# Kernel optimization log

Measured on AMD Instinct MI355X. Metric: run time of the kernel, lower is better.

The kernel has to match this reference:

```python
import jax, jax.numpy as jnp
import numpy as np

N_NODES = 100000   # number of graph nodes
DEG = 16           # fixed average degree
N_EDGES = N_NODES * DEG  # 1,600,000
D_FEAT = 48        # node feature dim


def setup_inputs() -> dict:
    key = jax.random.key(0)
    k1, k2 = jax.random.split(key)
    X = jax.random.normal(k1, (N_NODES, D_FEAT), dtype=jnp.float32)
    # CSR row offsets for a fixed-degree graph: row i owns edges [i*DEG, (i+1)*DEG)
    row_pointers = jnp.arange(N_NODES + 1, dtype=jnp.int32) * DEG
    # neighbor (source) node index per edge
    column_index = jax.random.randint(k2, (N_EDGES,), 0, N_NODES, dtype=jnp.int32)
    return {"X": X, "row_pointers": row_pointers, "column_index": column_index}


def reference(X, row_pointers, column_index):
    # Unweighted CSR SpMM neighbor aggregation (same math as TCGNN.forward SAG):
    #   out[i] = sum_{e in [row_ptr[i], row_ptr[i+1])} X[column_index[e]]
    n = row_pointers.shape[0] - 1
    e = column_index.shape[0]
    deg = jnp.diff(row_pointers)  # [n] edges per destination row
    # destination row id for every edge (static total length keeps this jit-able)
    row_ids = jnp.repeat(jnp.arange(n, dtype=jnp.int32), deg, total_repeat_length=e)
    gathered = X[column_index]  # [E, D] gather of neighbor features
    return jax.ops.segment_sum(gathered, row_ids, num_segments=n)  # [n, D]
```

## Files before the change

kernel.cpp:

```cpp
#include <hip/hip_runtime.h>


#define N_NODES 100000
#define DEG 16
#define NCHUNK (N_NODES * 4)

__global__ __launch_bounds__(256) void encode_kernel(
    const float4* __restrict__ X,
    uint4* __restrict__ Xq)
{
    int g = blockIdx.x * 256 + threadIdx.x;
    if (g >= NCHUNK) return;
    float4 a = X[g * 3 + 0];
    float4 b = X[g * 3 + 1];
    float4 d = X[g * 3 + 2];
    float x[12] = {a.x, a.y, a.z, a.w, b.x, b.y, b.z, b.w, d.x, d.y, d.z, d.w};

    float m = 0.f;
    #pragma unroll
    for (int j = 0; j < 12; ++j) m = fmaxf(m, fabsf(x[j]));

    int e;
    if (m > 0.f) {
        float t = m * (1.0f / 511.0f);
        e = (int)((__float_as_uint(t) >> 23) & 255u) - 126;
    } else {
        e = -64;
    }
    float inv_s = __uint_as_float((unsigned)(127 - e) << 23);
    unsigned code = (unsigned)(e + 64) & 255u;

    unsigned w[4];
    #pragma unroll
    for (int dw = 0; dw < 4; ++dw) {
        unsigned acc = 0u;
        #pragma unroll
        for (int k = 0; k < 3; ++k) {
            int q = __float2int_rn(x[dw * 3 + k] * inv_s);
            q = max(-511, min(511, q));
            acc |= ((unsigned)q & 1023u) << (10 * k);
        }
        acc |= ((code >> (2 * dw)) & 3u) << 30;
        w[dw] = acc;
    }
    uint4 o; o.x = w[0]; o.y = w[1]; o.z = w[2]; o.w = w[3];
    Xq[g] = o;
}

__global__ __launch_bounds__(256) void sag_q8_kernel(
    const uint4* __restrict__ Xq,
    const int* __restrict__ col,
    float4* __restrict__ out)
{
    const int t = threadIdx.x;
    const int node = blockIdx.x * 32 + (t >> 3);
    const int sub = t & 7;
    const int c = sub & 3;
    const int half = sub >> 2;
    if (node >= N_NODES) return;

    const int4* ip = (const int4*)(col + node * DEG + half * 8);
    int4 v0 = ip[0];
    int4 v1 = ip[1];
    int idx[8] = {v0.x, v0.y, v0.z, v0.w, v1.x, v1.y, v1.z, v1.w};

    uint4 w[8];
    #pragma unroll
    for (int k = 0; k < 8; ++k) {
        w[k] = Xq[((unsigned)idx[k] << 2) + c];
    }

    float acc[12];
    #pragma unroll
    for (int j = 0; j < 12; ++j) acc[j] = 0.f;

    #pragma unroll
    for (int k = 0; k < 8; ++k) {
        unsigned ws[4] = {w[k].x, w[k].y, w[k].z, w[k].w};
        unsigned code = (ws[0] >> 30) | ((ws[1] >> 30) << 2) |
                        ((ws[2] >> 30) << 4) | ((ws[3] >> 30) << 6);
        float s = __uint_as_float((code + 63u) << 23);
        #pragma unroll
        for (int dw = 0; dw < 4; ++dw) {
            unsigned wv = ws[dw];
            int q0 = ((int)(wv << 22)) >> 22;
            int q1 = ((int)(wv << 12)) >> 22;
            int q2 = ((int)(wv <<  2)) >> 22;
            acc[dw * 3 + 0] += (float)q0 * s;
            acc[dw * 3 + 1] += (float)q1 * s;
            acc[dw * 3 + 2] += (float)q2 * s;
        }
    }

    #pragma unroll
    for (int j = 0; j < 12; ++j) acc[j] += __shfl_xor(acc[j], 4);

    float4* o = out + ((long)node * 12 + c * 3);
    if (half == 0) {
        o[0] = make_float4(acc[0], acc[1],  acc[2],  acc[3]);
        o[1] = make_float4(acc[4], acc[5],  acc[6],  acc[7]);
    } else {
        o[2] = make_float4(acc[8], acc[9],  acc[10], acc[11]);
    }
}

__global__ __launch_bounds__(192) void sag_f32_kernel(
    const float4* __restrict__ X,
    const int* __restrict__ col,
    float4* __restrict__ out)
{
    const int t = threadIdx.x;
    const int node = blockIdx.x * 16 + t / 12;
    const int c = t % 12;
    if (node >= N_NODES) return;
    const int4* ip = (const int4*)(col + node * DEG);
    int idx[DEG];
    #pragma unroll
    for (int q = 0; q < 4; ++q) {
        int4 v = ip[q];
        idx[4 * q + 0] = v.x; idx[4 * q + 1] = v.y;
        idx[4 * q + 2] = v.z; idx[4 * q + 3] = v.w;
    }
    float4 acc = make_float4(0.f, 0.f, 0.f, 0.f);
    #pragma unroll
    for (int e = 0; e < DEG; ++e) {
        float4 v = X[idx[e] * 12 + c];
        acc.x += v.x; acc.y += v.y; acc.z += v.z; acc.w += v.w;
    }
    out[node * 12 + c] = acc;
}

extern "C" void kernel_launch(void* const* d_in, const int* in_sizes, int n_in,
                              void* d_out, int out_size, void* d_ws, size_t ws_size,
                              hipStream_t stream) {
    const float4* X = (const float4*)d_in[0];
    const int* col = (const int*)d_in[2];
    float4* out = (float4*)d_out;

    const size_t xq_bytes = (size_t)N_NODES * 64;

    if (ws_size >= xq_bytes) {
        uint4* Xq = (uint4*)d_ws;
        encode_kernel<<<(NCHUNK + 255) / 256, 256, 0, stream>>>(X, Xq);
        const int blocks = (N_NODES + 31) / 32;
        sag_q8_kernel<<<blocks, 256, 0, stream>>>(Xq, col, out);
    } else {
        const int blocks = (N_NODES + 15) / 16;
        sag_f32_kernel<<<blocks, 192, 0, stream>>>(X, col, out);
    }
}
```

Measured before the change: 95.66 us.

## Split quantized gather into two passes by source-node half for cache locality

The aggregation now runs in two launches: the first gathers only neighbors whose index falls in the lower half of the node range, and the second gathers the upper half and adds the first pass's partial sums read back from the output. The goal is to make each pass's random gather working set (half of the 6.4 MB encoded table) fit better in cache. Streaming loads and stores of the inputs, outputs and column indices are marked nontemporal. In exchange, the column indices are read twice, the output is written twice and read once more, and there is an extra launch.

```diff
diff --git a/kernel.cpp b/kernel.cpp
--- a/kernel.cpp
+++ b/kernel.cpp
@@ -4,16 +4,21 @@
 #define N_NODES 100000
 #define DEG 16
 #define NCHUNK (N_NODES * 4)
+#define HALF_SPLIT (N_NODES / 2)
+
+typedef float    f4 __attribute__((ext_vector_type(4)));
+typedef int      i4 __attribute__((ext_vector_type(4)));
+typedef unsigned u4 __attribute__((ext_vector_type(4)));
 
 __global__ __launch_bounds__(256) void encode_kernel(
-    const float4* __restrict__ X,
-    uint4* __restrict__ Xq)
+    const f4* __restrict__ X,
+    u4* __restrict__ Xq)
 {
     int g = blockIdx.x * 256 + threadIdx.x;
     if (g >= NCHUNK) return;
-    float4 a = X[g * 3 + 0];
-    float4 b = X[g * 3 + 1];
-    float4 d = X[g * 3 + 2];
+    f4 a = __builtin_nontemporal_load(X + g * 3 + 0);
+    f4 b = __builtin_nontemporal_load(X + g * 3 + 1);
+    f4 d = __builtin_nontemporal_load(X + g * 3 + 2);
     float x[12] = {a.x, a.y, a.z, a.w, b.x, b.y, b.z, b.w, d.x, d.y, d.z, d.w};
 
     float m = 0.f;
@@ -43,14 +48,15 @@
         acc |= ((code >> (2 * dw)) & 3u) << 30;
         w[dw] = acc;
     }
-    uint4 o; o.x = w[0]; o.y = w[1]; o.z = w[2]; o.w = w[3];
-    Xq[g] = o;
+    u4 o = {w[0], w[1], w[2], w[3]};
+    __builtin_nontemporal_store(o, Xq + g);
 }
 
-__global__ __launch_bounds__(256) void sag_q8_kernel(
-    const uint4* __restrict__ Xq,
+template<int H>
+__global__ __launch_bounds__(256) void sag_q8_pass(
+    const u4* __restrict__ Xq,
     const int* __restrict__ col,
-    float4* __restrict__ out)
+    f4* __restrict__ out)
 {
     const int t = threadIdx.x;
     const int node = blockIdx.x * 32 + (t >> 3);
@@ -59,15 +65,32 @@
     const int half = sub >> 2;
     if (node >= N_NODES) return;
 
-    const int4* ip = (const int4*)(col + node * DEG + half * 8);
-    int4 v0 = ip[0];
-    int4 v1 = ip[1];
+    f4* o = out + ((long)node * 12 + c * 3);
+
+    f4 p0 = {0.f, 0.f, 0.f, 0.f};
+    f4 p1 = p0, p2 = p0;
+    if (H == 1) {
+        if (half == 0) {
+            p0 = __builtin_nontemporal_load(o + 0);
+            p1 = __builtin_nontemporal_load(o + 1);
+        } else {
+            p2 = __builtin_nontemporal_load(o + 2);
+        }
+    }
+
+    const i4* ip = (const i4*)(col + node * DEG + half * 8);
+    i4 v0 = __builtin_nontemporal_load(ip + 0);
+    i4 v1 = __builtin_nontemporal_load(ip + 1);
     int idx[8] = {v0.x, v0.y, v0.z, v0.w, v1.x, v1.y, v1.z, v1.w};
 
-    uint4 w[8];
+    u4 w[8];
     #pragma unroll
     for (int k = 0; k < 8; ++k) {
-        w[k] = Xq[((unsigned)idx[k] << 2) + c];
+        u4 z = {0u, 0u, 0u, 0u};
+        w[k] = z;
+        const bool act = (H == 0) ? (idx[k] < HALF_SPLIT)
+                                  : (idx[k] >= HALF_SPLIT);
+        if (act) w[k] = Xq[((unsigned)idx[k] << 2) + c];
     }
 
     float acc[12];
@@ -95,12 +118,27 @@
     #pragma unroll
     for (int j = 0; j < 12; ++j) acc[j] += __shfl_xor(acc[j], 4);
 
-    float4* o = out + ((long)node * 12 + c * 3);
-    if (half == 0) {
-        o[0] = make_float4(acc[0], acc[1],  acc[2],  acc[3]);
-        o[1] = make_float4(acc[4], acc[5],  acc[6],  acc[7]);
+    if (H == 0) {
+        if (half == 0) {
+            f4 s0 = {acc[0], acc[1], acc[2], acc[3]};
+            f4 s1 = {acc[4], acc[5], acc[6], acc[7]};
+            __builtin_nontemporal_store(s0, o + 0);
+            __builtin_nontemporal_store(s1, o + 1);
+        } else {
+            f4 s2 = {acc[8], acc[9], acc[10], acc[11]};
+            __builtin_nontemporal_store(s2, o + 2);
+        }
     } else {
-        o[2] = make_float4(acc[8], acc[9],  acc[10], acc[11]);
+        if (half == 0) {
+            f4 s0 = {acc[0] + p0.x, acc[1] + p0.y, acc[2] + p0.z, acc[3] + p0.w};
+            f4 s1 = {acc[4] + p1.x, acc[5] + p1.y, acc[6] + p1.z, acc[7] + p1.w};
+            __builtin_nontemporal_store(s0, o + 0);
+            __builtin_nontemporal_store(s1, o + 1);
+        } else {
+            f4 s2 = {acc[8] + p2.x, acc[9] + p2.y,
+                     acc[10] + p2.z, acc[11] + p2.w};
+            __builtin_nontemporal_store(s2, o + 2);
+        }
     }
 }
 
@@ -133,19 +171,21 @@
 extern "C" void kernel_launch(void* const* d_in, const int* in_sizes, int n_in,
                               void* d_out, int out_size, void* d_ws, size_t ws_size,
                               hipStream_t stream) {
-    const float4* X = (const float4*)d_in[0];
+    const f4* X = (const f4*)d_in[0];
     const int* col = (const int*)d_in[2];
-    float4* out = (float4*)d_out;
+    f4* out = (f4*)d_out;
 
     const size_t xq_bytes = (size_t)N_NODES * 64;
 
     if (ws_size >= xq_bytes) {
-        uint4* Xq = (uint4*)d_ws;
+        u4* Xq = (u4*)d_ws;
         encode_kernel<<<(NCHUNK + 255) / 256, 256, 0, stream>>>(X, Xq);
         const int blocks = (N_NODES + 31) / 32;
-        sag_q8_kernel<<<blocks, 256, 0, stream>>>(Xq, col, out);
+        sag_q8_pass<0><<<blocks, 256, 0, stream>>>(Xq, col, out);
+        sag_q8_pass<1><<<blocks, 256, 0, stream>>>(Xq, col, out);
     } else {
         const int blocks = (N_NODES + 15) / 16;
-        sag_f32_kernel<<<blocks, 192, 0, stream>>>(X, col, out);
+        sag_f32_kernel<<<(N_NODES + 15) / 16, 192, 0, stream>>>(
+            (const float4*)d_in[0], col, (float4*)d_out);
     }
 }
```

Measured after the change: 160.0 us. +67.2%, slower.
